# Optimization experiments

Measured on AMD Instinct MI355X. Metric: run time of the kernel, lower is better.

Reference implementation:

```python
import jax, jax.numpy as jnp
import numpy as np

EPS = 1e-8

def setup_inputs() -> dict:
    key = jax.random.key(0)
    k1, k2 = jax.random.split(key)
    B, IN, OUT, G = 32768, 256, 256, 5
    x = jax.random.normal(k1, (B, IN), dtype=jnp.float32)
    grid = jnp.linspace(-1.0, 1.0, G).astype(jnp.float32)
    coef = jax.random.normal(k2, (OUT, IN, G), dtype=jnp.float32) * 0.1
    scale = jnp.ones((OUT, IN), dtype=jnp.float32)
    bias = jnp.zeros((OUT,), dtype=jnp.float32)
    return {"x": x, "grid": grid, "coef": coef, "scale": scale, "bias": bias}

def reference(x, grid, coef, scale, bias):
    # global min-max normalization to [-1, 1]
    xmin, xmax = x.min(), x.max()
    xn = 2.0 * (x - xmin) / (xmax - xmin + EPS) - 1.0
    # cubic bump B-spline-like basis: (batch, in, grid)
    dist = jnp.abs(xn[..., None] - grid)
    basis = jnp.where(dist < 1.0, 1.0 - dist ** 3, 0.0)
    basis = basis / (basis.sum(axis=-1, keepdims=True) + EPS)
    # fused contraction over (in, grid); equals ((basis*coef).sum(-1)*scale).sum(-1)
    w = coef * scale[..., None]          # (out, in, grid)
    out = jnp.einsum('big,oig->bo', basis, w) + bias
    return out
```

## Files before the change

### kernel.cpp

```cpp
#include <hip/hip_runtime.h>
#include <stdint.h>


#define B_SZ   32768
#define IN_SZ  256
#define OUT_SZ 256
#define EPSF   1e-8f
#define NMB    1536

typedef __bf16 bf16x8 __attribute__((ext_vector_type(8)));
typedef unsigned short ushort8 __attribute__((ext_vector_type(8)));
typedef float floatx16 __attribute__((ext_vector_type(16)));

union frag_u { uint4 u; bf16x8 v; };

__device__ __forceinline__ unsigned short f2bf(float f) {
  unsigned u = __float_as_uint(f);
  u += 0x7FFFu + ((u >> 16) & 1u);
  return (unsigned short)(u >> 16);
}


__global__ void __launch_bounds__(256) prep_kernel(const float* __restrict__ coef,
                                                   const float* __restrict__ scale,
                                                   const float* __restrict__ x,
                                                   unsigned short* __restrict__ wf,
                                                   float* __restrict__ part, int n4) {
  const int t = threadIdx.x;
  if (blockIdx.x < 256) {
    int idx = blockIdx.x * 256 + t;
    int o = idx >> 8, i = idx & 255;
    float s = scale[idx];
    const float* c = coef + (size_t)idx * 5;
    ushort8 v;
    v[0] = f2bf(c[0] * s); v[1] = f2bf(c[1] * s); v[2] = f2bf(c[2] * s);
    v[3] = f2bf(c[3] * s); v[4] = f2bf(c[4] * s);
    v[5] = 0; v[6] = 0; v[7] = 0;
    int chunk = (((o >> 5) * 64 + (i >> 2)) * 2 + ((i >> 1) & 1)) * 64
                + (i & 1) * 32 + (o & 31);
    *(ushort8*)(wf + (size_t)chunk * 8) = v;
  } else {
    int mb = blockIdx.x - 256;
    const float4* x4 = (const float4*)x;
    float lmin = 1e30f, lmax = -1e30f;
    for (int i = mb * 256 + t; i < n4; i += NMB * 256) {
      float4 v = x4[i];
      lmin = fminf(lmin, fminf(fminf(v.x, v.y), fminf(v.z, v.w)));
      lmax = fmaxf(lmax, fmaxf(fmaxf(v.x, v.y), fmaxf(v.z, v.w)));
    }
    #pragma unroll
    for (int off = 32; off >= 1; off >>= 1) {
      lmin = fminf(lmin, __shfl_down(lmin, off, 64));
      lmax = fmaxf(lmax, __shfl_down(lmax, off, 64));
    }
    __shared__ float smn[4], smx[4];
    if ((t & 63) == 0) { smn[t >> 6] = lmin; smx[t >> 6] = lmax; }
    __syncthreads();
    if (t == 0) {
      part[2 * mb]     = fminf(fminf(smn[0], smn[1]), fminf(smn[2], smn[3]));
      part[2 * mb + 1] = fmaxf(fmaxf(smx[0], smx[1]), fmaxf(smx[2], smx[3]));
    }
  }
}

__device__ __forceinline__ bf16x8 basisfrag(float xval, float scA, float scB) {
  float xn = fmaf(xval, scA, scB);
  float d0 = xn + 1.0f, d1 = xn + 0.5f, d3 = xn - 0.5f, d4 = xn - 1.0f;
  float b0 = fmaxf(fmaf(d0 * d0, -fabsf(d0), 1.0f), 0.0f);
  float b1 = fmaxf(fmaf(d1 * d1, -fabsf(d1), 1.0f), 0.0f);
  float b2 = fmaxf(fmaf(xn * xn, -fabsf(xn), 1.0f), 0.0f);
  float b3 = fmaxf(fmaf(d3 * d3, -fabsf(d3), 1.0f), 0.0f);
  float b4 = fmaxf(fmaf(d4 * d4, -fabsf(d4), 1.0f), 0.0f);
  float sum = ((b0 + b1) + (b2 + b3)) + b4;
  float inv = __builtin_amdgcn_rcpf(sum);
  b0 *= inv; b1 *= inv; b2 *= inv; b3 *= inv; b4 *= inv;
  frag_u r;
  r.u.x = __builtin_amdgcn_perm(__float_as_uint(b1), __float_as_uint(b0), 0x07060302u);
  r.u.y = __builtin_amdgcn_perm(__float_as_uint(b3), __float_as_uint(b2), 0x07060302u);
  r.u.z = __float_as_uint(b4) >> 16;
  r.u.w = 0u;
  return r.v;
}

__global__ void __launch_bounds__(256, 4) kan_gemm(
    const float* __restrict__ x,
    const unsigned short* __restrict__ wf,
    const float* __restrict__ bias,
    const float* __restrict__ part,
    float* __restrict__ out)
{
  __shared__ __align__(16) unsigned short Bb[2][8192];
  __shared__ float2 red[4];

  const int t = threadIdx.x;
  const int lane = t & 63;
  const int wm = t >> 6;
  const int l31 = lane & 31, lh = lane >> 5;
  const int bRow = blockIdx.x * 128;
  const int bCol = blockIdx.y * 64;
  const int row = bRow + wm * 32 + l31;

  auto stage = [&](int c, int buf) {
    #pragma unroll
    for (int r = 0; r < 4; ++r) {
      int idx = r * 4 + wm;
      const unsigned short* src = wf +
          ((size_t)(((blockIdx.y * 2 + (idx >> 3)) * 64 + (c * 4 + ((idx >> 1) & 3))) * 2
                    + (idx & 1))) * 512 + (size_t)lane * 8;
      __builtin_amdgcn_global_load_lds(
          (const __attribute__((address_space(1))) unsigned int*)src,
          (__attribute__((address_space(3))) unsigned int*)(&Bb[buf][idx * 512 + lane * 8]),
          16, 0, 0);
    }
  };

  const float* xrow = x + (size_t)row * IN_SZ;

  stage(0, 0);
  float4 xq[4], xqn[4];
  #pragma unroll
  for (int g = 0; g < 4; ++g) xq[g] = *(const float4*)(xrow + g * 4);

  float mn = 1e30f, mx = -1e30f;
  const float2* part2 = (const float2*)part;
  #pragma unroll
  for (int k = 0; k < NMB / 256; ++k) {
    float2 p = part2[k * 256 + t];
    mn = fminf(mn, p.x); mx = fmaxf(mx, p.y);
  }
  #pragma unroll
  for (int off = 32; off >= 1; off >>= 1) {
    mn = fminf(mn, __shfl_down(mn, off, 64));
    mx = fmaxf(mx, __shfl_down(mx, off, 64));
  }
  if (lane == 0) red[wm] = make_float2(mn, mx);
  __syncthreads();
  mn = fminf(fminf(red[0].x, red[1].x), fminf(red[2].x, red[3].x));
  mx = fmaxf(fmaxf(red[0].y, red[1].y), fmaxf(red[2].y, red[3].y));
  const float scA = 2.0f / (mx - mn + EPSF);
  const float scB = -mn * scA - 1.0f;

  floatx16 acc[2] = {};
  bf16x8 br[2][4];

  auto ldsB = [&](int ktr, int buf, bf16x8* dst) {
    #pragma unroll
    for (int q = 0; q < 4; ++q) {
      int ni = q >> 1, ks = q & 1;
      dst[q] = *(const bf16x8*)(&Bb[buf][((ni * 4 + ktr) * 2 + ks) * 512 + lane * 8]);
    }
  };

  for (int c = 0; c < 16; ++c) {
    const int buf = c & 1;

    if (c < 15) {
      #pragma unroll
      for (int g = 0; g < 4; ++g)
        xqn[g] = *(const float4*)(xrow + (c + 1) * 16 + g * 4);
      stage(c + 1, buf ^ 1);
    }
    __builtin_amdgcn_sched_barrier(0);
    if (c < 15) asm volatile("s_waitcnt vmcnt(8)");
    else        asm volatile("s_waitcnt vmcnt(0)");
    __builtin_amdgcn_s_barrier();
    __builtin_amdgcn_sched_barrier(0);

    ldsB(0, buf, br[0]);

    #pragma unroll
    for (int ktr = 0; ktr < 4; ++ktr) {
      if (ktr < 3) ldsB(ktr + 1, buf, br[(ktr + 1) & 1]);

      float xv0 = lh ? xq[ktr].y : xq[ktr].x;
      float xv1 = lh ? xq[ktr].w : xq[ktr].z;
      bf16x8 af0 = basisfrag(xv0, scA, scB);
      bf16x8 af1 = basisfrag(xv1, scA, scB);

      bf16x8* Bf = br[ktr & 1];
      __builtin_amdgcn_s_setprio(1);
      acc[0] = __builtin_amdgcn_mfma_f32_32x32x16_bf16(af0, Bf[0], acc[0], 0, 0, 0);
      acc[1] = __builtin_amdgcn_mfma_f32_32x32x16_bf16(af0, Bf[2], acc[1], 0, 0, 0);
      acc[0] = __builtin_amdgcn_mfma_f32_32x32x16_bf16(af1, Bf[1], acc[0], 0, 0, 0);
      acc[1] = __builtin_amdgcn_mfma_f32_32x32x16_bf16(af1, Bf[3], acc[1], 0, 0, 0);
      __builtin_amdgcn_s_setprio(0);
    }

    if (c < 15) {
      #pragma unroll
      for (int g = 0; g < 4; ++g) xq[g] = xqn[g];
      __builtin_amdgcn_sched_barrier(0);
      __builtin_amdgcn_s_barrier();
      __builtin_amdgcn_sched_barrier(0);
    }
  }

  #pragma unroll
  for (int ni = 0; ni < 2; ++ni) {
    int o = bCol + ni * 32 + l31;
    float bs = bias[o];
    int rb = bRow + wm * 32 + 4 * lh;
    #pragma unroll
    for (int reg = 0; reg < 16; ++reg) {
      int r = rb + (reg & 3) + 8 * (reg >> 2);
      out[(size_t)r * OUT_SZ + o] = acc[ni][reg] + bs;
    }
  }
}

extern "C" void kernel_launch(void* const* d_in, const int* in_sizes, int n_in,
                              void* d_out, int out_size, void* d_ws, size_t ws_size,
                              hipStream_t stream) {
  const float* x     = (const float*)d_in[0];
  const float* coef  = (const float*)d_in[2];
  const float* scale = (const float*)d_in[3];
  const float* bias  = (const float*)d_in[4];
  float* out = (float*)d_out;

  size_t need = 16384 + (size_t)OUT_SZ * IN_SZ * 8 * 2;
  if (ws_size < need) return;

  float* part = (float*)d_ws;
  unsigned short* wf = (unsigned short*)((char*)d_ws + 16384);

  prep_kernel<<<256 + NMB, 256, 0, stream>>>(coef, scale, x, wf, part,
                                             (B_SZ * IN_SZ) / 4);
  dim3 g(B_SZ / 128, OUT_SZ / 64);
  kan_gemm<<<g, 256, 0, stream>>>(x, wf, bias, part, out);
}
```

Baseline: 142.1 us.

## Enlarge GEMM block tile to 256x128 and fix min-max reduction trip count

Each block now covers 256 rows and 128 output columns, and every wave runs a 2x4 grid of 32x32 MFMA tiles instead of 1x2. This halves how many times each x row is loaded and turned into spline-basis fragments across column blocks, and halves redundant weight staging per output. The launch now has 256 blocks at one block per CU, so there is little occupancy left to hide latency, and register pressure goes up. The min-max prep pass gets more blocks and a fixed unrolled loop of four loads per thread.

New measurement: 145.4 us. +2.3%, slower.

```diff
diff --git a/kernel.cpp b/kernel.cpp
--- a/kernel.cpp
+++ b/kernel.cpp
@@ -6,7 +6,7 @@
 #define IN_SZ  256
 #define OUT_SZ 256
 #define EPSF   1e-8f
-#define NMB    1536
+#define NMB    2048
 
 typedef __bf16 bf16x8 __attribute__((ext_vector_type(8)));
 typedef unsigned short ushort8 __attribute__((ext_vector_type(8)));
@@ -42,9 +42,11 @@
   } else {
     int mb = blockIdx.x - 256;
     const float4* x4 = (const float4*)x;
+    int i = mb * 256 + t;
     float lmin = 1e30f, lmax = -1e30f;
-    for (int i = mb * 256 + t; i < n4; i += NMB * 256) {
-      float4 v = x4[i];
+    #pragma unroll
+    for (int k = 0; k < 4; ++k) {
+      float4 v = x4[i + k * (NMB * 256)];
       lmin = fminf(lmin, fminf(fminf(v.x, v.y), fminf(v.z, v.w)));
       lmax = fmaxf(lmax, fmaxf(fmaxf(v.x, v.y), fmaxf(v.z, v.w)));
     }
@@ -82,30 +84,30 @@
   return r.v;
 }
 
-__global__ void __launch_bounds__(256, 4) kan_gemm(
+__global__ void __launch_bounds__(256, 1) kan_gemm(
     const float* __restrict__ x,
     const unsigned short* __restrict__ wf,
     const float* __restrict__ bias,
     const float* __restrict__ part,
     float* __restrict__ out)
 {
-  __shared__ __align__(16) unsigned short Bb[2][8192];
+  __shared__ __align__(16) unsigned short Bb[2][16384];
   __shared__ float2 red[4];
 
   const int t = threadIdx.x;
   const int lane = t & 63;
   const int wm = t >> 6;
   const int l31 = lane & 31, lh = lane >> 5;
-  const int bRow = blockIdx.x * 128;
-  const int bCol = blockIdx.y * 64;
-  const int row = bRow + wm * 32 + l31;
+  const int bRow = blockIdx.x * 256;
+  const int bCol = blockIdx.y * 128;
+  const int row0 = bRow + wm * 64 + l31;
 
   auto stage = [&](int c, int buf) {
     #pragma unroll
-    for (int r = 0; r < 4; ++r) {
+    for (int r = 0; r < 8; ++r) {
       int idx = r * 4 + wm;
       const unsigned short* src = wf +
-          ((size_t)(((blockIdx.y * 2 + (idx >> 3)) * 64 + (c * 4 + ((idx >> 1) & 3))) * 2
+          ((size_t)(((blockIdx.y * 4 + (idx >> 3)) * 64 + (c * 4 + ((idx >> 1) & 3))) * 2
                     + (idx & 1))) * 512 + (size_t)lane * 8;
       __builtin_amdgcn_global_load_lds(
           (const __attribute__((address_space(1))) unsigned int*)src,
@@ -114,12 +116,16 @@
     }
   };
 
-  const float* xrow = x + (size_t)row * IN_SZ;
+  const float* xrow0 = x + (size_t)row0 * IN_SZ;
+  const float* xrow1 = xrow0 + 32 * IN_SZ;
 
   stage(0, 0);
-  float4 xq[4], xqn[4];
-  #pragma unroll
-  for (int g = 0; g < 4; ++g) xq[g] = *(const float4*)(xrow + g * 4);
+  float4 xq0[4], xq1[4], xqn0[4], xqn1[4];
+  #pragma unroll
+  for (int g = 0; g < 4; ++g) {
+    xq0[g] = *(const float4*)(xrow0 + g * 4);
+    xq1[g] = *(const float4*)(xrow1 + g * 4);
+  }
 
   float mn = 1e30f, mx = -1e30f;
   const float2* part2 = (const float2*)part;
@@ -140,12 +146,12 @@
   const float scA = 2.0f / (mx - mn + EPSF);
   const float scB = -mn * scA - 1.0f;
 
-  floatx16 acc[2] = {};
-  bf16x8 br[2][4];
+  floatx16 acc0[4] = {}, acc1[4] = {};
+  bf16x8 br[2][8];
 
   auto ldsB = [&](int ktr, int buf, bf16x8* dst) {
     #pragma unroll
-    for (int q = 0; q < 4; ++q) {
+    for (int q = 0; q < 8; ++q) {
       int ni = q >> 1, ks = q & 1;
       dst[q] = *(const bf16x8*)(&Bb[buf][((ni * 4 + ktr) * 2 + ks) * 512 + lane * 8]);
     }
@@ -156,12 +162,14 @@
 
     if (c < 15) {
       #pragma unroll
-      for (int g = 0; g < 4; ++g)
-        xqn[g] = *(const float4*)(xrow + (c + 1) * 16 + g * 4);
+      for (int g = 0; g < 4; ++g) {
+        xqn0[g] = *(const float4*)(xrow0 + (c + 1) * 16 + g * 4);
+        xqn1[g] = *(const float4*)(xrow1 + (c + 1) * 16 + g * 4);
+      }
       stage(c + 1, buf ^ 1);
     }
     __builtin_amdgcn_sched_barrier(0);
-    if (c < 15) asm volatile("s_waitcnt vmcnt(8)");
+    if (c < 15) asm volatile("s_waitcnt vmcnt(16)");
     else        asm volatile("s_waitcnt vmcnt(0)");
     __builtin_amdgcn_s_barrier();
     __builtin_amdgcn_sched_barrier(0);
@@ -172,23 +180,33 @@
     for (int ktr = 0; ktr < 4; ++ktr) {
       if (ktr < 3) ldsB(ktr + 1, buf, br[(ktr + 1) & 1]);
 
-      float xv0 = lh ? xq[ktr].y : xq[ktr].x;
-      float xv1 = lh ? xq[ktr].w : xq[ktr].z;
-      bf16x8 af0 = basisfrag(xv0, scA, scB);
-      bf16x8 af1 = basisfrag(xv1, scA, scB);
+      float xv00 = lh ? xq0[ktr].y : xq0[ktr].x;
+      float xv01 = lh ? xq0[ktr].w : xq0[ktr].z;
+      float xv10 = lh ? xq1[ktr].y : xq1[ktr].x;
+      float xv11 = lh ? xq1[ktr].w : xq1[ktr].z;
+      bf16x8 a00 = basisfrag(xv00, scA, scB);
+      bf16x8 a01 = basisfrag(xv01, scA, scB);
+      bf16x8 a10 = basisfrag(xv10, scA, scB);
+      bf16x8 a11 = basisfrag(xv11, scA, scB);
 
       bf16x8* Bf = br[ktr & 1];
       __builtin_amdgcn_s_setprio(1);
-      acc[0] = __builtin_amdgcn_mfma_f32_32x32x16_bf16(af0, Bf[0], acc[0], 0, 0, 0);
-      acc[1] = __builtin_amdgcn_mfma_f32_32x32x16_bf16(af0, Bf[2], acc[1], 0, 0, 0);
-      acc[0] = __builtin_amdgcn_mfma_f32_32x32x16_bf16(af1, Bf[1], acc[0], 0, 0, 0);
-      acc[1] = __builtin_amdgcn_mfma_f32_32x32x16_bf16(af1, Bf[3], acc[1], 0, 0, 0);
+      #pragma unroll
+      for (int ni = 0; ni < 4; ++ni) {
+        acc0[ni] = __builtin_amdgcn_mfma_f32_32x32x16_bf16(a00, Bf[ni * 2 + 0], acc0[ni], 0, 0, 0);
+        acc1[ni] = __builtin_amdgcn_mfma_f32_32x32x16_bf16(a10, Bf[ni * 2 + 0], acc1[ni], 0, 0, 0);
+      }
+      #pragma unroll
+      for (int ni = 0; ni < 4; ++ni) {
+        acc0[ni] = __builtin_amdgcn_mfma_f32_32x32x16_bf16(a01, Bf[ni * 2 + 1], acc0[ni], 0, 0, 0);
+        acc1[ni] = __builtin_amdgcn_mfma_f32_32x32x16_bf16(a11, Bf[ni * 2 + 1], acc1[ni], 0, 0, 0);
+      }
       __builtin_amdgcn_s_setprio(0);
     }
 
     if (c < 15) {
       #pragma unroll
-      for (int g = 0; g < 4; ++g) xq[g] = xqn[g];
+      for (int g = 0; g < 4; ++g) { xq0[g] = xqn0[g]; xq1[g] = xqn1[g]; }
       __builtin_amdgcn_sched_barrier(0);
       __builtin_amdgcn_s_barrier();
       __builtin_amdgcn_sched_barrier(0);
@@ -196,14 +214,15 @@
   }
 
   #pragma unroll
-  for (int ni = 0; ni < 2; ++ni) {
+  for (int ni = 0; ni < 4; ++ni) {
     int o = bCol + ni * 32 + l31;
     float bs = bias[o];
-    int rb = bRow + wm * 32 + 4 * lh;
+    int rb = bRow + wm * 64 + 4 * lh;
     #pragma unroll
     for (int reg = 0; reg < 16; ++reg) {
       int r = rb + (reg & 3) + 8 * (reg >> 2);
-      out[(size_t)r * OUT_SZ + o] = acc[ni][reg] + bs;
+      out[(size_t)r * OUT_SZ + o] = acc0[ni][reg] + bs;
+      out[(size_t)(r + 32) * OUT_SZ + o] = acc1[ni][reg] + bs;
     }
   }
 }
@@ -225,6 +244,6 @@
 
   prep_kernel<<<256 + NMB, 256, 0, stream>>>(coef, scale, x, wf, part,
                                              (B_SZ * IN_SZ) / 4);
-  dim3 g(B_SZ / 128, OUT_SZ / 64);
+  dim3 g(B_SZ / 256, OUT_SZ / 128);
   kan_gemm<<<g, 256, 0, stream>>>(x, wf, bias, part, out);
 }
```

## Switch GEMM to 16x16x32 MFMA with 64x128 block tiles and new weight layout

Applied to the files above, without the earlier changes.

Replaces the 32x32x16 MFMA tiling (128 rows x 64 cols per block) with 16x16x32 MFMAs over 64 rows x 128 cols, so each wave computes one basis fragment per input feature and reuses it across eight output sub-tiles. The packed weight layout and LDS staging are rearranged to match, and the K loop now steps over 8 inputs per stage for 32 iterations. The min/max pre-reduction also moves to 2048 blocks with a fixed 4-iteration unrolled loop. The aim is less redundant basis computation per MFMA and better load balance, at the cost of twice as many barriers and stage iterations and more, smaller output stores.

Result: no change. 143.4 us (+0.9%).

```diff
diff --git a/kernel.cpp b/kernel.cpp
--- a/kernel.cpp
+++ b/kernel.cpp
@@ -6,11 +6,11 @@
 #define IN_SZ  256
 #define OUT_SZ 256
 #define EPSF   1e-8f
-#define NMB    1536
+#define NMB    2048
 
 typedef __bf16 bf16x8 __attribute__((ext_vector_type(8)));
 typedef unsigned short ushort8 __attribute__((ext_vector_type(8)));
-typedef float floatx16 __attribute__((ext_vector_type(16)));
+typedef float floatx4 __attribute__((ext_vector_type(4)));
 
 union frag_u { uint4 u; bf16x8 v; };
 
@@ -36,15 +36,16 @@
     v[0] = f2bf(c[0] * s); v[1] = f2bf(c[1] * s); v[2] = f2bf(c[2] * s);
     v[3] = f2bf(c[3] * s); v[4] = f2bf(c[4] * s);
     v[5] = 0; v[6] = 0; v[7] = 0;
-    int chunk = (((o >> 5) * 64 + (i >> 2)) * 2 + ((i >> 1) & 1)) * 64
-                + (i & 1) * 32 + (o & 31);
-    *(ushort8*)(wf + (size_t)chunk * 8) = v;
+    int cb = o >> 4, om = o & 15;
+    *(ushort8*)(wf + ((size_t)((cb * 256 + i) * 16 + om)) * 8) = v;
   } else {
     int mb = blockIdx.x - 256;
     const float4* x4 = (const float4*)x;
+    int i = mb * 256 + t;
     float lmin = 1e30f, lmax = -1e30f;
-    for (int i = mb * 256 + t; i < n4; i += NMB * 256) {
-      float4 v = x4[i];
+    #pragma unroll
+    for (int k = 0; k < 4; ++k) {
+      float4 v = x4[i + k * (NMB * 256)];
       lmin = fminf(lmin, fminf(fminf(v.x, v.y), fminf(v.z, v.w)));
       lmax = fmaxf(lmax, fmaxf(fmaxf(v.x, v.y), fmaxf(v.z, v.w)));
     }
@@ -95,31 +96,31 @@
   const int t = threadIdx.x;
   const int lane = t & 63;
   const int wm = t >> 6;
-  const int l31 = lane & 31, lh = lane >> 5;
-  const int bRow = blockIdx.x * 128;
-  const int bCol = blockIdx.y * 64;
-  const int row = bRow + wm * 32 + l31;
+  const int l15 = lane & 15, koff = lane >> 4;
+  const int bRow = blockIdx.x * 64;
+  const int bCol = blockIdx.y * 128;
+  const int row = bRow + wm * 16 + l15;
 
   auto stage = [&](int c, int buf) {
     #pragma unroll
     for (int r = 0; r < 4; ++r) {
-      int idx = r * 4 + wm;
-      const unsigned short* src = wf +
-          ((size_t)(((blockIdx.y * 2 + (idx >> 3)) * 64 + (c * 4 + ((idx >> 1) & 3))) * 2
-                    + (idx & 1))) * 512 + (size_t)lane * 8;
+      int s = r * 4 + wm;
+      int cb = blockIdx.y * 8 + (s & 7);
+      int i0 = c * 8 + (s >> 3) * 4;
+      const unsigned short* src = wf + ((size_t)(cb * 256 + i0) * 16) * 8
+                                     + (size_t)lane * 8;
       __builtin_amdgcn_global_load_lds(
           (const __attribute__((address_space(1))) unsigned int*)src,
-          (__attribute__((address_space(3))) unsigned int*)(&Bb[buf][idx * 512 + lane * 8]),
+          (__attribute__((address_space(3))) unsigned int*)(&Bb[buf][s * 512 + lane * 8]),
           16, 0, 0);
     }
   };
 
   const float* xrow = x + (size_t)row * IN_SZ;
 
+  float xc0 = xrow[koff];
+  float xc1 = xrow[4 + koff];
   stage(0, 0);
-  float4 xq[4], xqn[4];
-  #pragma unroll
-  for (int g = 0; g < 4; ++g) xq[g] = *(const float4*)(xrow + g * 4);
 
   float mn = 1e30f, mx = -1e30f;
   const float2* part2 = (const float2*)part;
@@ -140,55 +141,51 @@
   const float scA = 2.0f / (mx - mn + EPSF);
   const float scB = -mn * scA - 1.0f;
 
-  floatx16 acc[2] = {};
-  bf16x8 br[2][4];
-
-  auto ldsB = [&](int ktr, int buf, bf16x8* dst) {
-    #pragma unroll
-    for (int q = 0; q < 4; ++q) {
-      int ni = q >> 1, ks = q & 1;
-      dst[q] = *(const bf16x8*)(&Bb[buf][((ni * 4 + ktr) * 2 + ks) * 512 + lane * 8]);
-    }
+  floatx4 acc[8] = {};
+  bf16x8 bf[8];
+
+  auto ldsB = [&](int ktr, int buf) {
+    #pragma unroll
+    for (int q = 0; q < 8; ++q)
+      bf[q] = *(const bf16x8*)(&Bb[buf][(ktr * 8 + q) * 512 + lane * 8]);
   };
 
-  for (int c = 0; c < 16; ++c) {
+  for (int c = 0; c < 32; ++c) {
     const int buf = c & 1;
-
-    if (c < 15) {
-      #pragma unroll
-      for (int g = 0; g < 4; ++g)
-        xqn[g] = *(const float4*)(xrow + (c + 1) * 16 + g * 4);
+    float xn0, xn1;
+
+    if (c < 31) {
+      xn0 = xrow[(c + 1) * 8 + koff];
+      xn1 = xrow[(c + 1) * 8 + 4 + koff];
       stage(c + 1, buf ^ 1);
     }
     __builtin_amdgcn_sched_barrier(0);
-    if (c < 15) asm volatile("s_waitcnt vmcnt(8)");
+    if (c < 31) asm volatile("s_waitcnt vmcnt(6)");
     else        asm volatile("s_waitcnt vmcnt(0)");
     __builtin_amdgcn_s_barrier();
     __builtin_amdgcn_sched_barrier(0);
 
-    ldsB(0, buf, br[0]);
-
-    #pragma unroll
-    for (int ktr = 0; ktr < 4; ++ktr) {
-      if (ktr < 3) ldsB(ktr + 1, buf, br[(ktr + 1) & 1]);
-
-      float xv0 = lh ? xq[ktr].y : xq[ktr].x;
-      float xv1 = lh ? xq[ktr].w : xq[ktr].z;
-      bf16x8 af0 = basisfrag(xv0, scA, scB);
-      bf16x8 af1 = basisfrag(xv1, scA, scB);
-
-      bf16x8* Bf = br[ktr & 1];
+    ldsB(0, buf);
+    {
+      bf16x8 a = basisfrag(xc0, scA, scB);
       __builtin_amdgcn_s_setprio(1);
-      acc[0] = __builtin_amdgcn_mfma_f32_32x32x16_bf16(af0, Bf[0], acc[0], 0, 0, 0);
-      acc[1] = __builtin_amdgcn_mfma_f32_32x32x16_bf16(af0, Bf[2], acc[1], 0, 0, 0);
-      acc[0] = __builtin_amdgcn_mfma_f32_32x32x16_bf16(af1, Bf[1], acc[0], 0, 0, 0);
-      acc[1] = __builtin_amdgcn_mfma_f32_32x32x16_bf16(af1, Bf[3], acc[1], 0, 0, 0);
+      #pragma unroll
+      for (int q = 0; q < 8; ++q)
+        acc[q] = __builtin_amdgcn_mfma_f32_16x16x32_bf16(a, bf[q], acc[q], 0, 0, 0);
       __builtin_amdgcn_s_setprio(0);
     }
-
-    if (c < 15) {
+    ldsB(1, buf);
+    {
+      bf16x8 a = basisfrag(xc1, scA, scB);
+      __builtin_amdgcn_s_setprio(1);
       #pragma unroll
-      for (int g = 0; g < 4; ++g) xq[g] = xqn[g];
+      for (int q = 0; q < 8; ++q)
+        acc[q] = __builtin_amdgcn_mfma_f32_16x16x32_bf16(a, bf[q], acc[q], 0, 0, 0);
+      __builtin_amdgcn_s_setprio(0);
+    }
+
+    if (c < 31) {
+      xc0 = xn0; xc1 = xn1;
       __builtin_amdgcn_sched_barrier(0);
       __builtin_amdgcn_s_barrier();
       __builtin_amdgcn_sched_barrier(0);
@@ -196,15 +193,13 @@
   }
 
   #pragma unroll
-  for (int ni = 0; ni < 2; ++ni) {
-    int o = bCol + ni * 32 + l31;
+  for (int q = 0; q < 8; ++q) {
+    int o = bCol + q * 16 + l15;
     float bs = bias[o];
-    int rb = bRow + wm * 32 + 4 * lh;
-    #pragma unroll
-    for (int reg = 0; reg < 16; ++reg) {
-      int r = rb + (reg & 3) + 8 * (reg >> 2);
-      out[(size_t)r * OUT_SZ + o] = acc[ni][reg] + bs;
-    }
+    int rb = bRow + wm * 16 + koff * 4;
+    #pragma unroll
+    for (int reg = 0; reg < 4; ++reg)
+      out[(size_t)(rb + reg) * OUT_SZ + o] = acc[q][reg] + bs;
   }
 }
 
@@ -225,6 +220,6 @@
 
   prep_kernel<<<256 + NMB, 256, 0, stream>>>(coef, scale, x, wf, part,
                                              (B_SZ * IN_SZ) / 4);
-  dim3 g(B_SZ / 128, OUT_SZ / 64);
+  dim3 g(B_SZ / 64, OUT_SZ / 128);
   kan_gemm<<<g, 256, 0, stream>>>(x, wf, bias, part, out);
 }
```
